# Optimization experiments

Measured on AMD Instinct MI355X. Metric: run time of the kernel, lower is better.

The kernel has to match this reference:

```python
import jax, jax.numpy as jnp
import numpy as np

R = 2            # interleaving factor (init kwarg r)
C = 16           # feature channels
N = 500_000      # number of sparse voxels
GRID = 256       # fine-grid extent per axis


def setup_inputs() -> dict:
    key = jax.random.key(0)
    kc, kf = jax.random.split(key)
    coords = jax.random.randint(kc, (N, 3), 0, GRID, dtype=jnp.int32)
    feats = jax.random.normal(kf, (N, C), dtype=jnp.float32)
    return {"feats": feats, "coords": coords}


def reference(feats, coords):
    # Sparse interleaving: group fine voxels into coarse voxels of size R^3,
    # scattering each point's C features into the slot given by its intra-cell offset.
    r2 = R * R
    r3 = r2 * R
    n = coords.shape[0]
    base = coords // R                      # [N,3] coarse voxel coords
    off = coords % R                        # [N,3] intra-cell offset
    offset_idx = off[:, 0] * r2 + off[:, 1] * R + off[:, 2]  # [N]

    # jit-compatible unique: fixed output size (worst case: all points distinct)
    unique_coords, inv = jnp.unique(base, axis=0, size=n, fill_value=-1,
                                    return_inverse=True)
    inv = inv.reshape(-1)                   # [N] row in aggregated output

    # target column = offset_idx*C + channel  (matches torch scatter_ layout)
    col = offset_idx[:, None] * C + jnp.arange(C, dtype=offset_idx.dtype)[None, :]  # [N,C]
    agg = jnp.zeros((n, C * r3), dtype=feats.dtype)
    agg = agg.at[inv[:, None], col].set(feats)
    return unique_coords.astype(jnp.int32), agg
```

## Files before the change

### kernel.cpp

```cpp
#include <hip/hip_runtime.h>


#define CELLS (1u << 21)
#define CHUNK 4096

__global__ void fill_coords_kernel(float* out, int n3) {
    int i = blockIdx.x * blockDim.x + threadIdx.x;
    if (i < n3) out[i] = -1.0f;
}

__global__ void mark_cells_kernel(const int* __restrict__ coords,
                                  unsigned* __restrict__ presence, int n) {
    int i = blockIdx.x * blockDim.x + threadIdx.x;
    if (i >= n) return;
    int cx = coords[3 * i], cy = coords[3 * i + 1], cz = coords[3 * i + 2];
    unsigned key = ((unsigned)(cx >> 1) << 14) | ((unsigned)(cy >> 1) << 7) |
                   (unsigned)(cz >> 1);
    presence[key] = 1u;
}

__global__ void scan1_kernel(const unsigned* __restrict__ presence,
                             unsigned* __restrict__ rank,
                             unsigned* __restrict__ blockSums) {
    __shared__ unsigned sh[256];
    int t = threadIdx.x;
    unsigned base = blockIdx.x * CHUNK + t * 16;
    unsigned v[16];
#pragma unroll
    for (int j = 0; j < 16; ++j) v[j] = presence[base + j];
    unsigned s = 0;
#pragma unroll
    for (int j = 0; j < 16; ++j) { unsigned x = v[j]; v[j] = s; s += x; }
    unsigned x = s;
    sh[t] = x; __syncthreads();
    for (int d = 1; d < 256; d <<= 1) {
        unsigned y = (t >= d) ? sh[t - d] : 0u;
        __syncthreads();
        x += y; sh[t] = x; __syncthreads();
    }
    unsigned excl = x - s;
#pragma unroll
    for (int j = 0; j < 16; ++j) rank[base + j] = v[j] + excl;
    if (t == 255) blockSums[blockIdx.x] = x;
}

__global__ void scan2_kernel(unsigned* blockSums) {
    __shared__ unsigned sh[512];
    int t = threadIdx.x;
    unsigned s = blockSums[t];
    unsigned x = s;
    sh[t] = x; __syncthreads();
    for (int d = 1; d < 512; d <<= 1) {
        unsigned y = (t >= d) ? sh[t - d] : 0u;
        __syncthreads();
        x += y; sh[t] = x; __syncthreads();
    }
    blockSums[t] = x - s;
}

__global__ void finalize_kernel(const unsigned* __restrict__ presence,
                                unsigned* __restrict__ rank,
                                const unsigned* __restrict__ blockSums,
                                float* __restrict__ coords_out) {
    unsigned i = blockIdx.x * 256 + threadIdx.x;
    unsigned r = rank[i] + blockSums[i >> 12];
    rank[i] = r;
    if (presence[i]) {
        coords_out[3 * r + 0] = (float)(i >> 14);
        coords_out[3 * r + 1] = (float)((i >> 7) & 127u);
        coords_out[3 * r + 2] = (float)(i & 127u);
    }
}

__global__ void pick_winner_kernel(const int* __restrict__ coords,
                                   const unsigned* __restrict__ rank,
                                   int* __restrict__ winner, int n) {
    int i = blockIdx.x * blockDim.x + threadIdx.x;
    if (i >= n) return;
    int cx = coords[3 * i], cy = coords[3 * i + 1], cz = coords[3 * i + 2];
    unsigned key = ((unsigned)(cx >> 1) << 14) | ((unsigned)(cy >> 1) << 7) |
                   (unsigned)(cz >> 1);
    unsigned off = ((unsigned)(cx & 1) << 2) | ((unsigned)(cy & 1) << 1) |
                   (unsigned)(cz & 1);
    atomicMax(&winner[rank[key] * 8u + off], i);
}

__global__ void scatter_kernel(const float* __restrict__ feats,
                               const int* __restrict__ coords,
                               const unsigned* __restrict__ rank,
                               const int* __restrict__ winner,
                               float* __restrict__ agg, int n) {
    int i = blockIdx.x * blockDim.x + threadIdx.x;
    if (i >= n) return;
    int cx = coords[3 * i], cy = coords[3 * i + 1], cz = coords[3 * i + 2];
    unsigned key = ((unsigned)(cx >> 1) << 14) | ((unsigned)(cy >> 1) << 7) |
                   (unsigned)(cz >> 1);
    unsigned off = ((unsigned)(cx & 1) << 2) | ((unsigned)(cy & 1) << 1) |
                   (unsigned)(cz & 1);
    unsigned r = rank[key];
    if (winner[r * 8u + off] != i) return;
    const float4* src = (const float4*)(feats + (size_t)i * 16);
    float4* dst = (float4*)(agg + (size_t)r * 128u + off * 16u);
    dst[0] = src[0]; dst[1] = src[1]; dst[2] = src[2]; dst[3] = src[3];
}

extern "C" void kernel_launch(void* const* d_in, const int* in_sizes, int n_in,
                              void* d_out, int out_size, void* d_ws, size_t ws_size,
                              hipStream_t stream) {
    const float* feats = (const float*)d_in[0];
    const int* coords  = (const int*)d_in[1];
    int n = in_sizes[1] / 3;

    float* out        = (float*)d_out;
    float* coords_out = out;
    float* agg        = out + (size_t)3 * n;

    unsigned* presence  = (unsigned*)d_ws;
    unsigned* rank      = presence + CELLS;
    unsigned* blockSums = rank + CELLS;
    int*      winner    = (int*)(blockSums + 1024);

    hipMemsetAsync(agg, 0, (size_t)128 * n * sizeof(float), stream);
    hipMemsetAsync(presence, 0, (size_t)CELLS * sizeof(unsigned), stream);
    hipMemsetAsync(winner, 0xFF, (size_t)8 * n * sizeof(int), stream);

    fill_coords_kernel<<<(3 * n + 255) / 256, 256, 0, stream>>>(coords_out, 3 * n);
    mark_cells_kernel<<<(n + 255) / 256, 256, 0, stream>>>(coords, presence, n);
    scan1_kernel<<<CELLS / CHUNK, 256, 0, stream>>>(presence, rank, blockSums);
    scan2_kernel<<<1, 512, 0, stream>>>(blockSums);
    finalize_kernel<<<CELLS / 256, 256, 0, stream>>>(presence, rank, blockSums,
                                                     coords_out);
    pick_winner_kernel<<<(n + 255) / 256, 256, 0, stream>>>(coords, rank, winner, n);
    scatter_kernel<<<(n + 255) / 256, 256, 0, stream>>>(feats, coords, rank, winner,
                                                        agg, n);
}
```

Measured before the change: 409.5 us.

## Use bit-packed occupancy with popcount ranks and a dense gather instead of memset+scatter

Replaces the 2M-entry presence/rank arrays with a 64K-word bitmap, where each cell's rank is its word's base rank plus a popcount of the lower bits. Coordinates are emitted per set bit, and the padding rows are written only past the unique count. The 256 MB agg memset plus the scattered writes are replaced by one coalesced gather pass that writes zeros or the winner's features into every slot. This cuts workspace traffic and removes the separate zero-fill of the large output, at the cost of per-word serial bit loops and atomicOr contention in the mark step.

```diff
diff --git a/kernel.cpp b/kernel.cpp
--- a/kernel.cpp
+++ b/kernel.cpp
@@ -1,36 +1,35 @@
 #include <hip/hip_runtime.h>
 
 
-#define CELLS (1u << 21)
-#define CHUNK 4096
+#define WORDS 65536u
 
-__global__ void fill_coords_kernel(float* out, int n3) {
-    int i = blockIdx.x * blockDim.x + threadIdx.x;
-    if (i < n3) out[i] = -1.0f;
-}
-
-__global__ void mark_cells_kernel(const int* __restrict__ coords,
-                                  unsigned* __restrict__ presence, int n) {
-    int i = blockIdx.x * blockDim.x + threadIdx.x;
+__global__ void mark_kernel(const int* __restrict__ coords,
+                            unsigned* __restrict__ bitmap, int n) {
+    int i = blockIdx.x * 256 + threadIdx.x;
     if (i >= n) return;
     int cx = coords[3 * i], cy = coords[3 * i + 1], cz = coords[3 * i + 2];
     unsigned key = ((unsigned)(cx >> 1) << 14) | ((unsigned)(cy >> 1) << 7) |
                    (unsigned)(cz >> 1);
-    presence[key] = 1u;
+    atomicOr(&bitmap[key >> 5], 1u << (key & 31));
 }
 
-__global__ void scan1_kernel(const unsigned* __restrict__ presence,
-                             unsigned* __restrict__ rank,
-                             unsigned* __restrict__ blockSums) {
+__global__ void chunksum_kernel(const unsigned* __restrict__ bitmap,
+                                unsigned* __restrict__ chunkSum) {
     __shared__ unsigned sh[256];
     int t = threadIdx.x;
-    unsigned base = blockIdx.x * CHUNK + t * 16;
-    unsigned v[16];
-#pragma unroll
-    for (int j = 0; j < 16; ++j) v[j] = presence[base + j];
-    unsigned s = 0;
-#pragma unroll
-    for (int j = 0; j < 16; ++j) { unsigned x = v[j]; v[j] = s; s += x; }
+    sh[t] = __popc(bitmap[blockIdx.x * 256 + t]);
+    __syncthreads();
+    for (int d = 128; d > 0; d >>= 1) {
+        if (t < d) sh[t] += sh[t + d];
+        __syncthreads();
+    }
+    if (t == 0) chunkSum[blockIdx.x] = sh[0];
+}
+
+__global__ void scan_kernel(unsigned* chunkSum, unsigned* U) {
+    __shared__ unsigned sh[256];
+    int t = threadIdx.x;
+    unsigned s = chunkSum[t];
     unsigned x = s;
     sh[t] = x; __syncthreads();
     for (int d = 1; d < 256; d <<= 1) {
@@ -38,70 +37,76 @@
         __syncthreads();
         x += y; sh[t] = x; __syncthreads();
     }
-    unsigned excl = x - s;
-#pragma unroll
-    for (int j = 0; j < 16; ++j) rank[base + j] = v[j] + excl;
-    if (t == 255) blockSums[blockIdx.x] = x;
+    chunkSum[t] = x - s;
+    if (t == 255) *U = x;
 }
 
-__global__ void scan2_kernel(unsigned* blockSums) {
-    __shared__ unsigned sh[512];
+__global__ void rank_coords_kernel(const unsigned* __restrict__ bitmap,
+                                   const unsigned* __restrict__ chunkExcl,
+                                   unsigned* __restrict__ rank_base,
+                                   float* __restrict__ coords_out) {
+    __shared__ unsigned sh[256];
     int t = threadIdx.x;
-    unsigned s = blockSums[t];
-    unsigned x = s;
+    unsigned w = blockIdx.x * 256 + t;
+    unsigned word = bitmap[w];
+    unsigned cnt = __popc(word);
+    unsigned x = cnt;
     sh[t] = x; __syncthreads();
-    for (int d = 1; d < 512; d <<= 1) {
+    for (int d = 1; d < 256; d <<= 1) {
         unsigned y = (t >= d) ? sh[t - d] : 0u;
         __syncthreads();
         x += y; sh[t] = x; __syncthreads();
     }
-    blockSums[t] = x - s;
-}
-
-__global__ void finalize_kernel(const unsigned* __restrict__ presence,
-                                unsigned* __restrict__ rank,
-                                const unsigned* __restrict__ blockSums,
-                                float* __restrict__ coords_out) {
-    unsigned i = blockIdx.x * 256 + threadIdx.x;
-    unsigned r = rank[i] + blockSums[i >> 12];
-    rank[i] = r;
-    if (presence[i]) {
-        coords_out[3 * r + 0] = (float)(i >> 14);
-        coords_out[3 * r + 1] = (float)((i >> 7) & 127u);
-        coords_out[3 * r + 2] = (float)(i & 127u);
+    unsigned rb = chunkExcl[blockIdx.x] + x - cnt;
+    rank_base[w] = rb;
+    while (word) {
+        int k = __ffs(word) - 1;
+        word &= word - 1;
+        unsigned cell = w * 32u + (unsigned)k;
+        coords_out[3 * rb + 0] = (float)(cell >> 14);
+        coords_out[3 * rb + 1] = (float)((cell >> 7) & 127u);
+        coords_out[3 * rb + 2] = (float)(cell & 127u);
+        ++rb;
     }
 }
 
-__global__ void pick_winner_kernel(const int* __restrict__ coords,
-                                   const unsigned* __restrict__ rank,
-                                   int* __restrict__ winner, int n) {
-    int i = blockIdx.x * blockDim.x + threadIdx.x;
+__global__ void pad_kernel(const unsigned* __restrict__ U,
+                           float* __restrict__ coords_out, int n) {
+    int i = blockIdx.x * 256 + threadIdx.x;
+    if (i < n && (unsigned)i >= *U) {
+        coords_out[3 * i + 0] = -1.0f;
+        coords_out[3 * i + 1] = -1.0f;
+        coords_out[3 * i + 2] = -1.0f;
+    }
+}
+
+__global__ void winner_kernel(const int* __restrict__ coords,
+                              const unsigned* __restrict__ bitmap,
+                              const unsigned* __restrict__ rank_base,
+                              int* __restrict__ winner, int n) {
+    int i = blockIdx.x * 256 + threadIdx.x;
     if (i >= n) return;
     int cx = coords[3 * i], cy = coords[3 * i + 1], cz = coords[3 * i + 2];
     unsigned key = ((unsigned)(cx >> 1) << 14) | ((unsigned)(cy >> 1) << 7) |
                    (unsigned)(cz >> 1);
     unsigned off = ((unsigned)(cx & 1) << 2) | ((unsigned)(cy & 1) << 1) |
                    (unsigned)(cz & 1);
-    atomicMax(&winner[rank[key] * 8u + off], i);
+    unsigned wd = key >> 5;
+    unsigned r = rank_base[wd] + __popc(bitmap[wd] & ((1u << (key & 31)) - 1u));
+    atomicMax(&winner[r * 8u + off], i);
 }
 
-__global__ void scatter_kernel(const float* __restrict__ feats,
-                               const int* __restrict__ coords,
-                               const unsigned* __restrict__ rank,
-                               const int* __restrict__ winner,
-                               float* __restrict__ agg, int n) {
-    int i = blockIdx.x * blockDim.x + threadIdx.x;
-    if (i >= n) return;
-    int cx = coords[3 * i], cy = coords[3 * i + 1], cz = coords[3 * i + 2];
-    unsigned key = ((unsigned)(cx >> 1) << 14) | ((unsigned)(cy >> 1) << 7) |
-                   (unsigned)(cz >> 1);
-    unsigned off = ((unsigned)(cx & 1) << 2) | ((unsigned)(cy & 1) << 1) |
-                   (unsigned)(cz & 1);
-    unsigned r = rank[key];
-    if (winner[r * 8u + off] != i) return;
-    const float4* src = (const float4*)(feats + (size_t)i * 16);
-    float4* dst = (float4*)(agg + (size_t)r * 128u + off * 16u);
-    dst[0] = src[0]; dst[1] = src[1]; dst[2] = src[2]; dst[3] = src[3];
+__global__ void gather_kernel(const float* __restrict__ feats,
+                              const int* __restrict__ winner,
+                              float* __restrict__ agg, int total4) {
+    int j = blockIdx.x * 256 + threadIdx.x;
+    if (j >= total4) return;
+    int slot = j >> 2;
+    int c4 = j & 3;
+    int w = winner[slot];
+    float4 v = make_float4(0.f, 0.f, 0.f, 0.f);
+    if (w >= 0) v = ((const float4*)feats)[(size_t)w * 4 + c4];
+    ((float4*)agg)[j] = v;
 }
 
 extern "C" void kernel_launch(void* const* d_in, const int* in_sizes, int n_in,
@@ -115,22 +120,24 @@
     float* coords_out = out;
     float* agg        = out + (size_t)3 * n;
 
-    unsigned* presence  = (unsigned*)d_ws;
-    unsigned* rank      = presence + CELLS;
-    unsigned* blockSums = rank + CELLS;
-    int*      winner    = (int*)(blockSums + 1024);
+    unsigned* bitmap    = (unsigned*)d_ws;
+    unsigned* rank_base = bitmap + WORDS;
+    unsigned* chunkSum  = rank_base + WORDS;
+    unsigned* U         = chunkSum + 256;
+    int*      winner    = (int*)(U + 4);
 
-    hipMemsetAsync(agg, 0, (size_t)128 * n * sizeof(float), stream);
-    hipMemsetAsync(presence, 0, (size_t)CELLS * sizeof(unsigned), stream);
+    hipMemsetAsync(bitmap, 0, WORDS * sizeof(unsigned), stream);
     hipMemsetAsync(winner, 0xFF, (size_t)8 * n * sizeof(int), stream);
 
-    fill_coords_kernel<<<(3 * n + 255) / 256, 256, 0, stream>>>(coords_out, 3 * n);
-    mark_cells_kernel<<<(n + 255) / 256, 256, 0, stream>>>(coords, presence, n);
-    scan1_kernel<<<CELLS / CHUNK, 256, 0, stream>>>(presence, rank, blockSums);
-    scan2_kernel<<<1, 512, 0, stream>>>(blockSums);
-    finalize_kernel<<<CELLS / 256, 256, 0, stream>>>(presence, rank, blockSums,
-                                                     coords_out);
-    pick_winner_kernel<<<(n + 255) / 256, 256, 0, stream>>>(coords, rank, winner, n);
-    scatter_kernel<<<(n + 255) / 256, 256, 0, stream>>>(feats, coords, rank, winner,
-                                                        agg, n);
+    int nb = (n + 255) / 256;
+    mark_kernel<<<nb, 256, 0, stream>>>(coords, bitmap, n);
+    chunksum_kernel<<<WORDS / 256, 256, 0, stream>>>(bitmap, chunkSum);
+    scan_kernel<<<1, 256, 0, stream>>>(chunkSum, U);
+    rank_coords_kernel<<<WORDS / 256, 256, 0, stream>>>(bitmap, chunkSum,
+                                                        rank_base, coords_out);
+    pad_kernel<<<nb, 256, 0, stream>>>(U, coords_out, n);
+    winner_kernel<<<nb, 256, 0, stream>>>(coords, bitmap, rank_base, winner, n);
+    int total4 = n * 32;
+    gather_kernel<<<(total4 + 255) / 256, 256, 0, stream>>>(feats, winner, agg,
+                                                            total4);
 }
```

Result: faster. 376.2 us (-8.1%).
